# Kernel optimization log

Hardware: AMD Instinct MI355X
Metric: run time of the kernel (lower is better)

The kernel has to match this reference:

```python
import jax, jax.numpy as jnp
import numpy as np

DIM, E, H, HS = 2048, 8, 1408, 2816
B, S = 4, 2048


def setup_inputs() -> dict:
    key = jax.random.key(0)
    ks = jax.random.split(key, 12)
    sc = 0.02
    return {
        "x": jax.random.normal(ks[0], (B, S, DIM), jnp.float32),
        "gate_w": jax.random.normal(ks[1], (E, DIM), jnp.float32) * sc,
        "gate_b": jnp.zeros((E,), jnp.float32),
        "w1": jax.random.normal(ks[2], (E, H, DIM), jnp.float32) * sc,
        "b1": jnp.zeros((E, H), jnp.float32),
        "w3": jax.random.normal(ks[3], (E, H, DIM), jnp.float32) * sc,
        "b3": jnp.zeros((E, H), jnp.float32),
        "w2": jax.random.normal(ks[4], (E, DIM, H), jnp.float32) * sc,
        "b2": jnp.zeros((E, DIM), jnp.float32),
        "sh_gate": jax.random.normal(ks[5], (HS, DIM), jnp.float32) * sc,
        "sh_up": jax.random.normal(ks[6], (HS, DIM), jnp.float32) * sc,
        "sh_down": jax.random.normal(ks[7], (DIM, HS), jnp.float32) * sc,
        "top_k": 2,
    }


def reference(x, gate_w, gate_b, w1, b1, w3, b3, w2, b2, sh_gate, sh_up, sh_down, top_k):
    shape = x.shape
    xt = x.reshape(-1, DIM)                       # [T, D]
    T = xt.shape[0]

    # Router: softmax -> top-k (bias is None so gathered weights == topk probs)
    logits = xt @ gate_w.T + gate_b               # [T, E]
    scores = jax.nn.softmax(logits, axis=-1)
    topk_w, topk_idx = jax.lax.top_k(scores, top_k)  # [T, K]
    # combine weights per (token, expert); topk indices are distinct per row
    combine = jnp.zeros((T, E), xt.dtype).at[jnp.arange(T)[:, None], topk_idx].add(topk_w)

    # Routed experts: dense batched SwiGLU over all experts, weighted combine.
    g = jax.nn.silu(jnp.einsum("td,ehd->teh", xt, w1) + b1)  # [T, E, H]
    u = jnp.einsum("td,ehd->teh", xt, w3) + b3               # [T, E, H]
    hw = (g * u) * combine[:, :, None]                        # weight before down-proj
    routed = jnp.einsum("teh,edh->td", hw, w2) + combine @ b2  # [T, D]

    # Shared expert (bias-free SwiGLU)
    shared = (jax.nn.silu(xt @ sh_gate.T) * (xt @ sh_up.T)) @ sh_down.T

    return (shared + routed).reshape(shape)
```

## Files before the change

kernel.cpp:

```cpp
#include <hip/hip_runtime.h>
#include <stdint.h>

#define DIM  2048
#define NEXP 8
#define NH   1408
#define NHS  2816
#define NT   8192
#define NA   (NT*2)

typedef unsigned short u16;
typedef short bf16x8 __attribute__((ext_vector_type(8)));
typedef float f32x4 __attribute__((ext_vector_type(4)));

typedef __attribute__((address_space(1))) const uint32_t gas_u32;
typedef __attribute__((address_space(3))) uint32_t las_u32;

__device__ __forceinline__ u16 f2bf(float f) {
  uint32_t x = __builtin_bit_cast(uint32_t, f);
  x += 0x7FFFu + ((x >> 16) & 1u);
  return (u16)(x >> 16);
}

__device__ __forceinline__ void gload_lds16(const void* g, void* l) {
  __builtin_amdgcn_global_load_lds((gas_u32*)g, (las_u32*)l, 16, 0, 0);
}

struct alignas(16) US8 { u16 u[8]; };

__global__ __launch_bounds__(256) void convert_kernel(const float* __restrict__ src,
                                                      u16* __restrict__ dst, int n8) {
  int i = blockIdx.x * 256 + threadIdx.x;
  if (i >= n8) return;
  const float4* s = (const float4*)src + (size_t)i * 2;
  float4 a = s[0], b = s[1];
  US8 r;
  r.u[0]=f2bf(a.x); r.u[1]=f2bf(a.y); r.u[2]=f2bf(a.z); r.u[3]=f2bf(a.w);
  r.u[4]=f2bf(b.x); r.u[5]=f2bf(b.y); r.u[6]=f2bf(b.z); r.u[7]=f2bf(b.w);
  *((US8*)dst + i) = r;
}

__global__ void zero_counts(int* counts) { if (threadIdx.x < NEXP) counts[threadIdx.x] = 0; }

__global__ __launch_bounds__(64) void router_kernel(const float* __restrict__ x,
    const float* __restrict__ gw, const float* __restrict__ gb,
    int* __restrict__ tope, float* __restrict__ topw, int* __restrict__ counts) {
  const int t = blockIdx.x;
  const int lane = threadIdx.x;
  const float4* xr = (const float4*)(x + (size_t)t * DIM);
  float4 xv[8];
  #pragma unroll
  for (int j = 0; j < 8; j++) xv[j] = xr[j * 64 + lane];
  float p[NEXP];
  #pragma unroll
  for (int e = 0; e < NEXP; e++) {
    const float4* gr = (const float4*)(gw + (size_t)e * DIM);
    float s = 0.f;
    #pragma unroll
    for (int j = 0; j < 8; j++) {
      float4 g = gr[j * 64 + lane];
      s += xv[j].x*g.x + xv[j].y*g.y + xv[j].z*g.z + xv[j].w*g.w;
    }
    p[e] = s;
  }
  #pragma unroll
  for (int off = 32; off > 0; off >>= 1) {
    #pragma unroll
    for (int e = 0; e < NEXP; e++) p[e] += __shfl_xor(p[e], off);
  }
  if (lane == 0) {
    float pr[NEXP];
    float mx = -1e30f;
    #pragma unroll
    for (int e = 0; e < NEXP; e++) { p[e] += gb[e]; mx = fmaxf(mx, p[e]); }
    float den = 0.f;
    #pragma unroll
    for (int e = 0; e < NEXP; e++) { pr[e] = __expf(p[e] - mx); den += pr[e]; }
    float inv = 1.f / den;
    #pragma unroll
    for (int e = 0; e < NEXP; e++) pr[e] *= inv;
    int e0 = 0;
    #pragma unroll
    for (int e = 1; e < NEXP; e++) if (pr[e] > pr[e0]) e0 = e;
    int e1 = (e0 == 0) ? 1 : 0;
    #pragma unroll
    for (int e = 0; e < NEXP; e++) { if (e != e0 && pr[e] > pr[e1]) e1 = e; }
    tope[t*2]   = e0; tope[t*2+1] = e1;
    topw[t*2]   = pr[e0]; topw[t*2+1] = pr[e1];
    atomicAdd(&counts[e0], 1); atomicAdd(&counts[e1], 1);
  }
}

__global__ void scan_kernel(const int* __restrict__ counts, int* __restrict__ offsets,
                            int* __restrict__ cursor) {
  if (threadIdx.x == 0) {
    int s = 0;
    for (int e = 0; e < NEXP; e++) { offsets[e] = s; cursor[e] = s; s += counts[e]; }
    offsets[NEXP] = s;
  }
}

__global__ __launch_bounds__(256) void assign_kernel(const int* __restrict__ tope,
    const float* __restrict__ topw, int* __restrict__ cursor,
    int* __restrict__ ptok, float* __restrict__ pw) {
  int t = blockIdx.x * 256 + threadIdx.x;
  if (t >= NT) return;
  #pragma unroll
  for (int k = 0; k < 2; k++) {
    int e = tope[t*2+k];
    int pos = atomicAdd(&cursor[e], 1);
    ptok[pos] = t;
    pw[pos]   = topw[t*2+k];
  }
}

template<bool ROUTED>
__global__ __launch_bounds__(256, 2) void gemm_up(
    const u16* __restrict__ X,
    const u16* __restrict__ Wg,
    const u16* __restrict__ Wu,
    const float* __restrict__ Bg,
    const float* __restrict__ Bu,
    u16* __restrict__ Hout,
    const int* __restrict__ offsets,
    const int* __restrict__ ptok,
    const float* __restrict__ pw,
    int Nfeat)
{
  const int nt = blockIdx.x;
  const int mt = blockIdx.y;
  int e = 0, seg = 0, cnt = NT;
  if (ROUTED) {
    e = blockIdx.z;
    seg = offsets[e];
    cnt = offsets[e+1] - seg;
    if (mt * 128 >= cnt) return;
  }
  const int m0 = mt * 128;
  const int tid = threadIdx.x;
  const int wave = tid >> 6, lane = tid & 63;

  __shared__ u16 sA[128*64];
  __shared__ u16 sBg[64*64];
  __shared__ u16 sBu[64*64];
  char* sAc  = (char*)sA;
  char* sBgc = (char*)sBg;
  char* sBuc = (char*)sBu;

  const u16* aSrc[4];
  #pragma unroll
  for (int j = 0; j < 4; j++) {
    int c = j * 256 + tid;
    int row = c >> 3, gch = (c & 7) ^ (row & 7);
    int r = m0 + row;
    size_t srow;
    if (ROUTED) { r = (r < cnt) ? r : (cnt - 1); srow = (size_t)ptok[seg + r]; }
    else        { srow = (size_t)r; }
    aSrc[j] = X + srow * DIM + gch * 8;
  }
  const size_t wOff = ROUTED ? (size_t)e * Nfeat * DIM : 0;
  const u16 *bgSrc[2], *buSrc[2];
  #pragma unroll
  for (int j = 0; j < 2; j++) {
    int c = j * 256 + tid;
    int row = c >> 3, gch = (c & 7) ^ (row & 7);
    bgSrc[j] = Wg + wOff + (size_t)(nt * 64 + row) * DIM + gch * 8;
    buSrc[j] = Wu + wOff + (size_t)(nt * 64 + row) * DIM + gch * 8;
  }

  f32x4 accg[4][2], accu[4][2];
  #pragma unroll
  for (int m = 0; m < 4; m++)
    #pragma unroll
    for (int n = 0; n < 2; n++) { accg[m][n] = (f32x4){0,0,0,0}; accu[m][n] = (f32x4){0,0,0,0}; }

  const int wr = (wave >> 1) * 64;
  const int wc = (wave & 1) * 32;
  const int lr = lane & 15, kg = lane >> 4;
  int aOff[4], bOff[2];
  #pragma unroll
  for (int m = 0; m < 4; m++) { int row = wr + m*16 + lr; aOff[m] = row*128 + ((kg ^ (row & 7)) & 7) * 16; }
  #pragma unroll
  for (int n = 0; n < 2; n++) { int row = wc + n*16 + lr; bOff[n] = row*128 + ((kg ^ (row & 7)) & 7) * 16; }

  for (int k0 = 0; k0 < DIM; k0 += 64) {
    __syncthreads();
    #pragma unroll
    for (int j = 0; j < 4; j++) gload_lds16(aSrc[j] + k0, sAc + j*4096 + wave*1024);
    #pragma unroll
    for (int j = 0; j < 2; j++) {
      gload_lds16(bgSrc[j] + k0, sBgc + j*4096 + wave*1024);
      gload_lds16(buSrc[j] + k0, sBuc + j*4096 + wave*1024);
    }
    __syncthreads();
    bf16x8 af[4][2], bgf[2][2], buf2[2][2];
    #pragma unroll
    for (int m = 0; m < 4; m++) {
      af[m][0] = *(const bf16x8*)(sAc + aOff[m]);
      af[m][1] = *(const bf16x8*)(sAc + (aOff[m] ^ 64));
    }
    #pragma unroll
    for (int n = 0; n < 2; n++) {
      bgf[n][0]  = *(const bf16x8*)(sBgc + bOff[n]);
      bgf[n][1]  = *(const bf16x8*)(sBgc + (bOff[n] ^ 64));
      buf2[n][0] = *(const bf16x8*)(sBuc + bOff[n]);
      buf2[n][1] = *(const bf16x8*)(sBuc + (bOff[n] ^ 64));
    }
    #pragma unroll
    for (int kk = 0; kk < 2; kk++)
      #pragma unroll
      for (int m = 0; m < 4; m++)
        #pragma unroll
        for (int n = 0; n < 2; n++) {
          accg[m][n] = __builtin_amdgcn_mfma_f32_16x16x32_bf16(af[m][kk], bgf[n][kk],  accg[m][n], 0, 0, 0);
          accu[m][n] = __builtin_amdgcn_mfma_f32_16x16x32_bf16(af[m][kk], buf2[n][kk], accu[m][n], 0, 0, 0);
        }
  }

  const int col0 = nt * 64 + wc;
  #pragma unroll
  for (int m = 0; m < 4; m++) {
    #pragma unroll
    for (int n = 0; n < 2; n++) {
      #pragma unroll
      for (int i = 0; i < 4; i++) {
        int rl = wr + m*16 + (lane >> 4) * 4 + i;
        int gr = m0 + rl;
        if (ROUTED && gr >= cnt) continue;
        int col = col0 + n*16 + (lane & 15);
        float g = accg[m][n][i];
        float u = accu[m][n][i];
        float scale = 1.f;
        size_t orow;
        if (ROUTED) {
          int ai = seg + gr;
          scale = pw[ai];
          g += Bg[e * Nfeat + col];
          u += Bu[e * Nfeat + col];
          orow = (size_t)ai;
        } else {
          orow = (size_t)gr;
        }
        float s = g / (1.f + __expf(-g));
        Hout[orow * (size_t)Nfeat + col] = f2bf(s * u * scale);
      }
    }
  }
}

template<bool ROUTED>
__global__ __launch_bounds__(256, 2) void gemm_down(
    const u16* __restrict__ Hin,
    const u16* __restrict__ W,
    const float* __restrict__ B2,
    float* __restrict__ Out,
    const int* __restrict__ offsets,
    const int* __restrict__ ptok,
    const float* __restrict__ pw,
    int Kdim)
{
  const int nt = blockIdx.x;
  const int mt = blockIdx.y;
  int e = 0, seg = 0, cnt = NT;
  if (ROUTED) {
    e = blockIdx.z;
    seg = offsets[e];
    cnt = offsets[e+1] - seg;
    if (mt * 128 >= cnt) return;
  }
  const int m0 = mt * 128;
  const int tid = threadIdx.x;
  const int wave = tid >> 6, lane = tid & 63;

  __shared__ u16 sA[128*64];
  __shared__ u16 sB[128*64];
  char* sAc = (char*)sA;
  char* sBc = (char*)sB;

  const u16* aSrc[4]; const u16* bSrc[4];
  #pragma unroll
  for (int j = 0; j < 4; j++) {
    int c = j * 256 + tid;
    int row = c >> 3, gch = (c & 7) ^ (row & 7);
    int r = m0 + row;
    size_t arow;
    if (ROUTED) { r = (r < cnt) ? r : (cnt - 1); arow = (size_t)(seg + r); }
    else        { arow = (size_t)r; }
    aSrc[j] = Hin + arow * (size_t)Kdim + gch * 8;
    size_t brow = (size_t)(ROUTED ? e * DIM : 0) + nt * 128 + row;
    bSrc[j] = W + brow * (size_t)Kdim + gch * 8;
  }

  f32x4 acc[4][4];
  #pragma unroll
  for (int m = 0; m < 4; m++)
    #pragma unroll
    for (int n = 0; n < 4; n++) acc[m][n] = (f32x4){0,0,0,0};

  const int wr = (wave >> 1) * 64, wc = (wave & 1) * 64;
  const int lr = lane & 15, kg = lane >> 4;
  int aOff[4], bOff[4];
  #pragma unroll
  for (int m = 0; m < 4; m++) { int row = wr + m*16 + lr; aOff[m] = row*128 + ((kg ^ (row & 7)) & 7) * 16; }
  #pragma unroll
  for (int n = 0; n < 4; n++) { int row = wc + n*16 + lr; bOff[n] = row*128 + ((kg ^ (row & 7)) & 7) * 16; }

  for (int k0 = 0; k0 < Kdim; k0 += 64) {
    __syncthreads();
    #pragma unroll
    for (int j = 0; j < 4; j++) {
      gload_lds16(aSrc[j] + k0, sAc + j*4096 + wave*1024);
      gload_lds16(bSrc[j] + k0, sBc + j*4096 + wave*1024);
    }
    __syncthreads();
    bf16x8 af[4][2], bf[4][2];
    #pragma unroll
    for (int m = 0; m < 4; m++) {
      af[m][0] = *(const bf16x8*)(sAc + aOff[m]);
      af[m][1] = *(const bf16x8*)(sAc + (aOff[m] ^ 64));
    }
    #pragma unroll
    for (int n = 0; n < 4; n++) {
      bf[n][0] = *(const bf16x8*)(sBc + bOff[n]);
      bf[n][1] = *(const bf16x8*)(sBc + (bOff[n] ^ 64));
    }
    #pragma unroll
    for (int kk = 0; kk < 2; kk++)
      #pragma unroll
      for (int m = 0; m < 4; m++)
        #pragma unroll
        for (int n = 0; n < 4; n++)
          acc[m][n] = __builtin_amdgcn_mfma_f32_16x16x32_bf16(af[m][kk], bf[n][kk], acc[m][n], 0, 0, 0);
  }

  const int col0 = nt * 128 + wc;
  #pragma unroll
  for (int m = 0; m < 4; m++) {
    #pragma unroll
    for (int n = 0; n < 4; n++) {
      #pragma unroll
      for (int i = 0; i < 4; i++) {
        int rl = wr + m*16 + (lane >> 4) * 4 + i;
        int gr = m0 + rl;
        int col = col0 + n*16 + (lane & 15);
        float v = acc[m][n][i];
        if (ROUTED) {
          if (gr < cnt) {
            int ai = seg + gr;
            int token = ptok[ai];
            float w = pw[ai];
            atomicAdd(Out + (size_t)token * DIM + col, v + w * B2[e * DIM + col]);
          }
        } else {
          Out[(size_t)gr * DIM + col] = v;
        }
      }
    }
  }
}

extern "C" void kernel_launch(void* const* d_in, const int* in_sizes, int n_in,
                              void* d_out, int out_size, void* d_ws, size_t ws_size,
                              hipStream_t stream) {
  (void)in_sizes; (void)n_in; (void)out_size; (void)ws_size;
  const float* x      = (const float*)d_in[0];
  const float* gate_w = (const float*)d_in[1];
  const float* gate_b = (const float*)d_in[2];
  const float* w1     = (const float*)d_in[3];
  const float* b1     = (const float*)d_in[4];
  const float* w3     = (const float*)d_in[5];
  const float* b3     = (const float*)d_in[6];
  const float* w2     = (const float*)d_in[7];
  const float* b2     = (const float*)d_in[8];
  const float* shg    = (const float*)d_in[9];
  const float* shu    = (const float*)d_in[10];
  const float* shd    = (const float*)d_in[11];
  float* out = (float*)d_out;

  char* ws = (char*)d_ws;
  size_t off = 0;
  auto alloc = [&](size_t bytes) -> void* {
    void* p = ws + off;
    off += (bytes + 255) & ~(size_t)255;
    return p;
  };
  u16* xb    = (u16*)alloc((size_t)NT * DIM * 2);
  u16* w1b   = (u16*)alloc((size_t)NEXP * NH * DIM * 2);
  u16* w3b   = (u16*)alloc((size_t)NEXP * NH * DIM * 2);
  u16* w2b   = (u16*)alloc((size_t)NEXP * DIM * NH * 2);
  u16* shgb  = (u16*)alloc((size_t)NHS * DIM * 2);
  u16* shub  = (u16*)alloc((size_t)NHS * DIM * 2);
  u16* shdb  = (u16*)alloc((size_t)DIM * NHS * 2);
  u16* hsh   = (u16*)alloc((size_t)NT * NHS * 2);
  u16* hr    = (u16*)alloc((size_t)NA * NH * 2);
  int*   tope    = (int*)alloc(NT * 2 * 4);
  float* topw    = (float*)alloc(NT * 2 * 4);
  int*   ptok    = (int*)alloc(NA * 4);
  float* pw      = (float*)alloc(NA * 4);
  int*   counts  = (int*)alloc(64);
  int*   offsets = (int*)alloc(64);
  int*   cursor  = (int*)alloc(64);

  auto cvt = [&](const float* s, u16* d, size_t n) {
    int n8 = (int)(n / 8);
    convert_kernel<<<(n8 + 255) / 256, 256, 0, stream>>>(s, d, n8);
  };
  cvt(x,   xb,   (size_t)NT * DIM);
  cvt(w1,  w1b,  (size_t)NEXP * NH * DIM);
  cvt(w3,  w3b,  (size_t)NEXP * NH * DIM);
  cvt(w2,  w2b,  (size_t)NEXP * DIM * NH);
  cvt(shg, shgb, (size_t)NHS * DIM);
  cvt(shu, shub, (size_t)NHS * DIM);
  cvt(shd, shdb, (size_t)DIM * NHS);

  zero_counts<<<1, 64, 0, stream>>>(counts);
  router_kernel<<<NT, 64, 0, stream>>>(x, gate_w, gate_b, tope, topw, counts);
  scan_kernel<<<1, 1, 0, stream>>>(counts, offsets, cursor);
  assign_kernel<<<NT / 256, 256, 0, stream>>>(tope, topw, cursor, ptok, pw);

  gemm_up<false><<<dim3(NHS / 64, NT / 128, 1), 256, 0, stream>>>(
      xb, shgb, shub, nullptr, nullptr, hsh, nullptr, nullptr, nullptr, NHS);
  gemm_up<true><<<dim3(NH / 64, NT / 128, NEXP), 256, 0, stream>>>(
      xb, w1b, w3b, b1, b3, hr, offsets, ptok, pw, NH);
  gemm_down<false><<<dim3(DIM / 128, NT / 128, 1), 256, 0, stream>>>(
      hsh, shdb, nullptr, out, nullptr, nullptr, nullptr, NHS);
  gemm_down<true><<<dim3(DIM / 128, NT / 128, NEXP), 256, 0, stream>>>(
      hr, w2b, b2, out, offsets, ptok, pw, NH);
}
```

Before: 1.123 ms.

## Double-buffer LDS tiles in up/down GEMMs and fuse x conversion into router

```diff
diff --git a/kernel.cpp b/kernel.cpp
--- a/kernel.cpp
+++ b/kernel.cpp
@@ -26,6 +26,7 @@
 }
 
 struct alignas(16) US8 { u16 u[8]; };
+struct alignas(8)  US4 { u16 u[4]; };
 
 __global__ __launch_bounds__(256) void convert_kernel(const float* __restrict__ src,
                                                       u16* __restrict__ dst, int n8) {
@@ -43,6 +44,7 @@
 
 __global__ __launch_bounds__(64) void router_kernel(const float* __restrict__ x,
     const float* __restrict__ gw, const float* __restrict__ gb,
+    u16* __restrict__ xb,
     int* __restrict__ tope, float* __restrict__ topw, int* __restrict__ counts) {
   const int t = blockIdx.x;
   const int lane = threadIdx.x;
@@ -50,6 +52,14 @@
   float4 xv[8];
   #pragma unroll
   for (int j = 0; j < 8; j++) xv[j] = xr[j * 64 + lane];
+  US4* xrow = (US4*)(xb + (size_t)t * DIM);
+  #pragma unroll
+  for (int j = 0; j < 8; j++) {
+    US4 r4;
+    r4.u[0] = f2bf(xv[j].x); r4.u[1] = f2bf(xv[j].y);
+    r4.u[2] = f2bf(xv[j].z); r4.u[3] = f2bf(xv[j].w);
+    xrow[j * 64 + lane] = r4;
+  }
   float p[NEXP];
   #pragma unroll
   for (int e = 0; e < NEXP; e++) {
@@ -139,9 +149,9 @@
   const int tid = threadIdx.x;
   const int wave = tid >> 6, lane = tid & 63;
 
-  __shared__ u16 sA[128*64];
-  __shared__ u16 sBg[64*64];
-  __shared__ u16 sBu[64*64];
+  __shared__ u16 sA[2*128*64];
+  __shared__ u16 sBg[2*64*64];
+  __shared__ u16 sBu[2*64*64];
   char* sAc  = (char*)sA;
   char* sBgc = (char*)sBg;
   char* sBuc = (char*)sBu;
@@ -182,28 +192,34 @@
   #pragma unroll
   for (int n = 0; n < 2; n++) { int row = wc + n*16 + lr; bOff[n] = row*128 + ((kg ^ (row & 7)) & 7) * 16; }
 
-  for (int k0 = 0; k0 < DIM; k0 += 64) {
+#define STAGE_UP(b, kt) { int k0_ = (kt) * 64; \
+  _Pragma("unroll") for (int j = 0; j < 4; j++) \
+    gload_lds16(aSrc[j] + k0_, sAc + (b)*16384 + j*4096 + wave*1024); \
+  _Pragma("unroll") for (int j = 0; j < 2; j++) { \
+    gload_lds16(bgSrc[j] + k0_, sBgc + (b)*8192 + j*4096 + wave*1024); \
+    gload_lds16(buSrc[j] + k0_, sBuc + (b)*8192 + j*4096 + wave*1024); } }
+
+  const int NKT = DIM / 64;
+  STAGE_UP(0, 0);
+  for (int t = 0; t < NKT; t++) {
     __syncthreads();
-    #pragma unroll
-    for (int j = 0; j < 4; j++) gload_lds16(aSrc[j] + k0, sAc + j*4096 + wave*1024);
-    #pragma unroll
-    for (int j = 0; j < 2; j++) {
-      gload_lds16(bgSrc[j] + k0, sBgc + j*4096 + wave*1024);
-      gload_lds16(buSrc[j] + k0, sBuc + j*4096 + wave*1024);
-    }
-    __syncthreads();
+    const int b = t & 1;
+    if (t + 1 < NKT) STAGE_UP(b ^ 1, t + 1);
+    const char* sa = sAc  + b * 16384;
+    const char* sg = sBgc + b * 8192;
+    const char* su = sBuc + b * 8192;
     bf16x8 af[4][2], bgf[2][2], buf2[2][2];
     #pragma unroll
     for (int m = 0; m < 4; m++) {
-      af[m][0] = *(const bf16x8*)(sAc + aOff[m]);
-      af[m][1] = *(const bf16x8*)(sAc + (aOff[m] ^ 64));
+      af[m][0] = *(const bf16x8*)(sa + aOff[m]);
+      af[m][1] = *(const bf16x8*)(sa + (aOff[m] ^ 64));
     }
     #pragma unroll
     for (int n = 0; n < 2; n++) {
-      bgf[n][0]  = *(const bf16x8*)(sBgc + bOff[n]);
-      bgf[n][1]  = *(const bf16x8*)(sBgc + (bOff[n] ^ 64));
-      buf2[n][0] = *(const bf16x8*)(sBuc + bOff[n]);
-      buf2[n][1] = *(const bf16x8*)(sBuc + (bOff[n] ^ 64));
+      bgf[n][0]  = *(const bf16x8*)(sg + bOff[n]);
+      bgf[n][1]  = *(const bf16x8*)(sg + (bOff[n] ^ 64));
+      buf2[n][0] = *(const bf16x8*)(su + bOff[n]);
+      buf2[n][1] = *(const bf16x8*)(su + (bOff[n] ^ 64));
     }
     #pragma unroll
     for (int kk = 0; kk < 2; kk++)
@@ -215,6 +231,7 @@
           accu[m][n] = __builtin_amdgcn_mfma_f32_16x16x32_bf16(af[m][kk], buf2[n][kk], accu[m][n], 0, 0, 0);
         }
   }
+#undef STAGE_UP
 
   const int col0 = nt * 64 + wc;
   #pragma unroll
@@ -271,8 +288,8 @@
   const int tid = threadIdx.x;
   const int wave = tid >> 6, lane = tid & 63;
 
-  __shared__ u16 sA[128*64];
-  __shared__ u16 sB[128*64];
+  __shared__ u16 sA[2*128*64];
+  __shared__ u16 sB[2*128*64];
   char* sAc = (char*)sA;
   char* sBc = (char*)sB;
 
@@ -304,24 +321,29 @@
   #pragma unroll
   for (int n = 0; n < 4; n++) { int row = wc + n*16 + lr; bOff[n] = row*128 + ((kg ^ (row & 7)) & 7) * 16; }
 
-  for (int k0 = 0; k0 < Kdim; k0 += 64) {
+#define STAGE_DN(b, kt) { int k0_ = (kt) * 64; \
+  _Pragma("unroll") for (int j = 0; j < 4; j++) { \
+    gload_lds16(aSrc[j] + k0_, sAc + (b)*16384 + j*4096 + wave*1024); \
+    gload_lds16(bSrc[j] + k0_, sBc + (b)*16384 + j*4096 + wave*1024); } }
+
+  const int NKT = Kdim / 64;
+  STAGE_DN(0, 0);
+  for (int t = 0; t < NKT; t++) {
     __syncthreads();
-    #pragma unroll
-    for (int j = 0; j < 4; j++) {
-      gload_lds16(aSrc[j] + k0, sAc + j*4096 + wave*1024);
-      gload_lds16(bSrc[j] + k0, sBc + j*4096 + wave*1024);
-    }
-    __syncthreads();
+    const int b = t & 1;
+    if (t + 1 < NKT) STAGE_DN(b ^ 1, t + 1);
+    const char* sa = sAc + b * 16384;
+    const char* sb = sBc + b * 16384;
     bf16x8 af[4][2], bf[4][2];
     #pragma unroll
     for (int m = 0; m < 4; m++) {
-      af[m][0] = *(const bf16x8*)(sAc + aOff[m]);
-      af[m][1] = *(const bf16x8*)(sAc + (aOff[m] ^ 64));
+      af[m][0] = *(const bf16x8*)(sa + aOff[m]);
+      af[m][1] = *(const bf16x8*)(sa + (aOff[m] ^ 64));
     }
     #pragma unroll
     for (int n = 0; n < 4; n++) {
-      bf[n][0] = *(const bf16x8*)(sBc + bOff[n]);
-      bf[n][1] = *(const bf16x8*)(sBc + (bOff[n] ^ 64));
+      bf[n][0] = *(const bf16x8*)(sb + bOff[n]);
+      bf[n][1] = *(const bf16x8*)(sb + (bOff[n] ^ 64));
     }
     #pragma unroll
     for (int kk = 0; kk < 2; kk++)
@@ -331,6 +353,7 @@
         for (int n = 0; n < 4; n++)
           acc[m][n] = __builtin_amdgcn_mfma_f32_16x16x32_bf16(af[m][kk], bf[n][kk], acc[m][n], 0, 0, 0);
   }
+#undef STAGE_DN
 
   const int col0 = nt * 128 + wc;
   #pragma unroll
@@ -404,7 +427,6 @@
     int n8 = (int)(n / 8);
     convert_kernel<<<(n8 + 255) / 256, 256, 0, stream>>>(s, d, n8);
   };
-  cvt(x,   xb,   (size_t)NT * DIM);
   cvt(w1,  w1b,  (size_t)NEXP * NH * DIM);
   cvt(w3,  w3b,  (size_t)NEXP * NH * DIM);
   cvt(w2,  w2b,  (size_t)NEXP * DIM * NH);
@@ -413,7 +435,7 @@
   cvt(shd, shdb, (size_t)DIM * NHS);
 
   zero_counts<<<1, 64, 0, stream>>>(counts);
-  router_kernel<<<NT, 64, 0, stream>>>(x, gate_w, gate_b, tope, topw, counts);
+  router_kernel<<<NT, 64, 0, stream>>>(x, gate_w, gate_b, xb, tope, topw, counts);
   scan_kernel<<<1, 1, 0, stream>>>(counts, offsets, cursor);
   assign_kernel<<<NT / 256, 256, 0, stream>>>(tope, topw, cursor, ptok, pw);
 
```

New measurement: 1.387 ms. 1.24x slower.

## Interleave gate/up weights and use 256x256 pipelined up-projection GEMM

Applied to the files above, without the earlier changes.

```diff
diff --git a/kernel.cpp b/kernel.cpp
--- a/kernel.cpp
+++ b/kernel.cpp
@@ -26,6 +26,7 @@
 }
 
 struct alignas(16) US8 { u16 u[8]; };
+struct alignas(8)  US4 { u16 u[4]; };
 
 __global__ __launch_bounds__(256) void convert_kernel(const float* __restrict__ src,
                                                       u16* __restrict__ dst, int n8) {
@@ -39,10 +40,24 @@
   *((US8*)dst + i) = r;
 }
 
+__global__ __launch_bounds__(256) void convert_ilv(const float* __restrict__ src,
+                                                   u16* __restrict__ dst, int n8, int par) {
+  int i = blockIdx.x * 256 + threadIdx.x;
+  if (i >= n8) return;
+  int row = i >> 8, c = i & 255;
+  const float4* s = (const float4*)src + (size_t)i * 2;
+  float4 a = s[0], b = s[1];
+  US8 r;
+  r.u[0]=f2bf(a.x); r.u[1]=f2bf(a.y); r.u[2]=f2bf(a.z); r.u[3]=f2bf(a.w);
+  r.u[4]=f2bf(b.x); r.u[5]=f2bf(b.y); r.u[6]=f2bf(b.z); r.u[7]=f2bf(b.w);
+  *((US8*)dst + (((size_t)(2*row + par)) << 8) + c) = r;
+}
+
 __global__ void zero_counts(int* counts) { if (threadIdx.x < NEXP) counts[threadIdx.x] = 0; }
 
 __global__ __launch_bounds__(64) void router_kernel(const float* __restrict__ x,
     const float* __restrict__ gw, const float* __restrict__ gb,
+    u16* __restrict__ xb,
     int* __restrict__ tope, float* __restrict__ topw, int* __restrict__ counts) {
   const int t = blockIdx.x;
   const int lane = threadIdx.x;
@@ -50,6 +65,14 @@
   float4 xv[8];
   #pragma unroll
   for (int j = 0; j < 8; j++) xv[j] = xr[j * 64 + lane];
+  US4* xrow = (US4*)(xb + (size_t)t * DIM);
+  #pragma unroll
+  for (int j = 0; j < 8; j++) {
+    US4 r4;
+    r4.u[0] = f2bf(xv[j].x); r4.u[1] = f2bf(xv[j].y);
+    r4.u[2] = f2bf(xv[j].z); r4.u[3] = f2bf(xv[j].w);
+    xrow[j * 64 + lane] = r4;
+  }
   float p[NEXP];
   #pragma unroll
   for (int e = 0; e < NEXP; e++) {
@@ -113,150 +136,157 @@
   }
 }
 
-template<bool ROUTED>
-__global__ __launch_bounds__(256, 2) void gemm_up(
-    const u16* __restrict__ X,
-    const u16* __restrict__ Wg,
-    const u16* __restrict__ Wu,
-    const float* __restrict__ Bg,
-    const float* __restrict__ Bu,
-    u16* __restrict__ Hout,
-    const int* __restrict__ offsets,
-    const int* __restrict__ ptok,
-    const float* __restrict__ pw,
-    int Nfeat)
+#define BAR() { asm volatile("" ::: "memory"); __builtin_amdgcn_s_barrier(); asm volatile("" ::: "memory"); }
+#define VM6 asm volatile("s_waitcnt vmcnt(6)" ::: "memory")
+#define VM0 asm volatile("s_waitcnt vmcnt(0)" ::: "memory")
+
+template<int EPI>
+__global__ __launch_bounds__(512, 2) void gemm8(
+    const u16* __restrict__ A, const u16* __restrict__ Bw, u16* __restrict__ Hout,
+    const float* __restrict__ biasG, const float* __restrict__ biasU,
+    const int* __restrict__ offsets, const int* __restrict__ ptok,
+    const float* __restrict__ pw, int M, int N, int K, int Hf)
 {
-  const int nt = blockIdx.x;
-  const int mt = blockIdx.y;
-  int e = 0, seg = 0, cnt = NT;
-  if (ROUTED) {
-    e = blockIdx.z;
-    seg = offsets[e];
-    cnt = offsets[e+1] - seg;
-    if (mt * 128 >= cnt) return;
-  }
-  const int m0 = mt * 128;
-  const int tid = threadIdx.x;
-  const int wave = tid >> 6, lane = tid & 63;
-
-  __shared__ u16 sA[128*64];
-  __shared__ u16 sBg[64*64];
-  __shared__ u16 sBu[64*64];
-  char* sAc  = (char*)sA;
-  char* sBgc = (char*)sBg;
-  char* sBuc = (char*)sBu;
-
-  const u16* aSrc[4];
-  #pragma unroll
-  for (int j = 0; j < 4; j++) {
-    int c = j * 256 + tid;
-    int row = c >> 3, gch = (c & 7) ^ (row & 7);
-    int r = m0 + row;
-    size_t srow;
-    if (ROUTED) { r = (r < cnt) ? r : (cnt - 1); srow = (size_t)ptok[seg + r]; }
-    else        { srow = (size_t)r; }
-    aSrc[j] = X + srow * DIM + gch * 8;
-  }
-  const size_t wOff = ROUTED ? (size_t)e * Nfeat * DIM : 0;
-  const u16 *bgSrc[2], *buSrc[2];
-  #pragma unroll
-  for (int j = 0; j < 2; j++) {
-    int c = j * 256 + tid;
-    int row = c >> 3, gch = (c & 7) ^ (row & 7);
-    bgSrc[j] = Wg + wOff + (size_t)(nt * 64 + row) * DIM + gch * 8;
-    buSrc[j] = Wu + wOff + (size_t)(nt * 64 + row) * DIM + gch * 8;
-  }
-
-  f32x4 accg[4][2], accu[4][2];
-  #pragma unroll
-  for (int m = 0; m < 4; m++)
-    #pragma unroll
-    for (int n = 0; n < 2; n++) { accg[m][n] = (f32x4){0,0,0,0}; accu[m][n] = (f32x4){0,0,0,0}; }
-
-  const int wr = (wave >> 1) * 64;
-  const int wc = (wave & 1) * 32;
-  const int lr = lane & 15, kg = lane >> 4;
-  int aOff[4], bOff[2];
-  #pragma unroll
-  for (int m = 0; m < 4; m++) { int row = wr + m*16 + lr; aOff[m] = row*128 + ((kg ^ (row & 7)) & 7) * 16; }
-  #pragma unroll
-  for (int n = 0; n < 2; n++) { int row = wc + n*16 + lr; bOff[n] = row*128 + ((kg ^ (row & 7)) & 7) * 16; }
-
-  for (int k0 = 0; k0 < DIM; k0 += 64) {
-    __syncthreads();
-    #pragma unroll
-    for (int j = 0; j < 4; j++) gload_lds16(aSrc[j] + k0, sAc + j*4096 + wave*1024);
-    #pragma unroll
-    for (int j = 0; j < 2; j++) {
-      gload_lds16(bgSrc[j] + k0, sBgc + j*4096 + wave*1024);
-      gload_lds16(buSrc[j] + k0, sBuc + j*4096 + wave*1024);
-    }
-    __syncthreads();
-    bf16x8 af[4][2], bgf[2][2], buf2[2][2];
-    #pragma unroll
-    for (int m = 0; m < 4; m++) {
-      af[m][0] = *(const bf16x8*)(sAc + aOff[m]);
-      af[m][1] = *(const bf16x8*)(sAc + (aOff[m] ^ 64));
-    }
-    #pragma unroll
-    for (int n = 0; n < 2; n++) {
-      bgf[n][0]  = *(const bf16x8*)(sBgc + bOff[n]);
-      bgf[n][1]  = *(const bf16x8*)(sBgc + (bOff[n] ^ 64));
-      buf2[n][0] = *(const bf16x8*)(sBuc + bOff[n]);
-      buf2[n][1] = *(const bf16x8*)(sBuc + (bOff[n] ^ 64));
-    }
-    #pragma unroll
-    for (int kk = 0; kk < 2; kk++)
+  constexpr bool SEG = (EPI == 1);
+  extern __shared__ char smem[];
+  const int nt = blockIdx.x, mt = blockIdx.y;
+  int e = 0, seg = 0, cnt = M;
+  if (SEG) { e = blockIdx.z; seg = offsets[e]; cnt = offsets[e+1] - seg; if (mt*256 >= cnt) return; }
+  const int tid = threadIdx.x, wave = tid >> 6, lane = tid & 63;
+  const int NKT = K >> 6;
+
+  const u16* Bp = Bw + (SEG ? (size_t)e * (size_t)N * K : (size_t)0);
+  const u16* sAp[2][2]; const u16* sBp[2][2];
+  {
+    const int trow = tid >> 3;
+    const int tch  = (tid & 7) ^ (trow & 7);
+    #pragma unroll
+    for (int h = 0; h < 2; h++)
       #pragma unroll
-      for (int m = 0; m < 4; m++)
-        #pragma unroll
-        for (int n = 0; n < 2; n++) {
-          accg[m][n] = __builtin_amdgcn_mfma_f32_16x16x32_bf16(af[m][kk], bgf[n][kk],  accg[m][n], 0, 0, 0);
-          accu[m][n] = __builtin_amdgcn_mfma_f32_16x16x32_bf16(af[m][kk], buf2[n][kk], accu[m][n], 0, 0, 0);
-        }
-  }
-
-  const int col0 = nt * 64 + wc;
-  #pragma unroll
-  for (int m = 0; m < 4; m++) {
-    #pragma unroll
-    for (int n = 0; n < 2; n++) {
+      for (int j = 0; j < 2; j++) {
+        int r = mt*256 + h*128 + j*64 + trow;
+        if (SEG) r = (r < cnt) ? r : (cnt - 1);
+        size_t arow = SEG ? (size_t)ptok[seg + r] : (size_t)r;
+        sAp[h][j] = A + arow * (size_t)K + tch * 8;
+        int br = nt*256 + h*128 + j*64 + trow;
+        sBp[h][j] = Bp + (size_t)br * K + tch * 8;
+      }
+  }
+
+  const int wm = wave >> 2, wn = wave & 3, hb = wn >> 1;
+  const int ln15 = lane & 15, kg = lane >> 4;
+  const int c0 = (kg ^ (ln15 & 7)) << 4;
+  const char* Ab0 = smem + ((0*2 + wm) << 14);
+  const char* Ab1 = smem + ((1*2 + wm) << 14);
+  const char* Bb0 = smem + 65536 + ((0*2 + hb) << 14);
+  const char* Bb1 = smem + 65536 + ((1*2 + hb) << 14);
+  const int arow0 = ln15 * 128;
+  const int brow0 = ((wn & 1) * 64 + ln15) * 128;
+
+  f32x4 acc[8][4];
+  #pragma unroll
+  for (int m = 0; m < 8; m++)
+    #pragma unroll
+    for (int n = 0; n < 4; n++) acc[m][n] = (f32x4){0,0,0,0};
+
+  bf16x8 fa[4][2], fb[4][2];
+
+#define STA(buf,h,kt) { size_t k_ = (size_t)(kt) * 64; \
+  gload_lds16(sAp[h][0] + k_, smem + (((buf)*2+(h))<<14) + wave*1024); \
+  gload_lds16(sAp[h][1] + k_, smem + (((buf)*2+(h))<<14) + 8192 + wave*1024); }
+#define STB(buf,h,kt) { size_t k_ = (size_t)(kt) * 64; \
+  gload_lds16(sBp[h][0] + k_, smem + 65536 + (((buf)*2+(h))<<14) + wave*1024); \
+  gload_lds16(sBp[h][1] + k_, smem + 65536 + (((buf)*2+(h))<<14) + 8192 + wave*1024); }
+#define LDFA(AB, qm) { _Pragma("unroll") for (int m_ = 0; m_ < 4; m_++) { \
+  const char* p_ = (AB) + (qm)*8192 + m_*2048 + arow0; \
+  fa[m_][0] = *(const bf16x8*)(p_ + c0); fa[m_][1] = *(const bf16x8*)(p_ + (c0 ^ 64)); } }
+#define LDFB(BB) { _Pragma("unroll") for (int n_ = 0; n_ < 4; n_++) { \
+  const char* p_ = (BB) + n_*2048 + brow0; \
+  fb[n_][0] = *(const bf16x8*)(p_ + c0); fb[n_][1] = *(const bf16x8*)(p_ + (c0 ^ 64)); } }
+#define PH(qm, n0) { __builtin_amdgcn_s_setprio(1); \
+  _Pragma("unroll") for (int kk_ = 0; kk_ < 2; kk_++) \
+  _Pragma("unroll") for (int m_ = 0; m_ < 4; m_++) \
+  _Pragma("unroll") for (int n_ = 0; n_ < 2; n_++) \
+    acc[(qm)*4+m_][(n0)+n_] = __builtin_amdgcn_mfma_f32_16x16x32_bf16( \
+        fa[m_][kk_], fb[(n0)+n_][kk_], acc[(qm)*4+m_][(n0)+n_], 0, 0, 0); \
+  __builtin_amdgcn_s_setprio(0); }
+
+  STB(0,0,0); STB(0,1,0); STA(0,0,0); STA(0,1,0);
+  STB(1,0,1); STB(1,1,1); STA(1,0,1);
+  VM6; BAR();
+
+  for (int t = 0; t < NKT; t += 2) {
+    const bool last = (t + 2 >= NKT);
+    LDFB(Bb0); LDFA(Ab0, 0);
+    STA(1,1,t+1);
+    PH(0,0);
+    BAR();
+    if (!last) STB(0,0,t+2);
+    PH(0,2);
+    BAR();
+    LDFA(Ab0, 1);
+    if (!last) STB(0,1,t+2);
+    PH(1,2);
+    BAR();
+    if (!last) { STA(0,0,t+2); VM6; } else { VM0; }
+    PH(1,0);
+    BAR();
+    LDFB(Bb1); LDFA(Ab1, 0);
+    if (!last) STA(0,1,t+2);
+    PH(0,0);
+    BAR();
+    if (!last) STB(1,0,t+3);
+    PH(0,2);
+    BAR();
+    LDFA(Ab1, 1);
+    if (!last) STB(1,1,t+3);
+    PH(1,2);
+    BAR();
+    if (!last) { STA(1,0,t+3); VM6; }
+    PH(1,0);
+    BAR();
+  }
+
+  #pragma unroll
+  for (int mi = 0; mi < 8; mi++) {
+    #pragma unroll
+    for (int ni = 0; ni < 4; ni++) {
+      int colC = nt*256 + wn*64 + ni*16 + ln15;
+      int h = colC >> 1;
+      int par = ln15 & 1;
       #pragma unroll
       for (int i = 0; i < 4; i++) {
-        int rl = wr + m*16 + (lane >> 4) * 4 + i;
-        int gr = m0 + rl;
-        if (ROUTED && gr >= cnt) continue;
-        int col = col0 + n*16 + (lane & 15);
-        float g = accg[m][n][i];
-        float u = accu[m][n][i];
-        float scale = 1.f;
-        size_t orow;
-        if (ROUTED) {
-          int ai = seg + gr;
-          scale = pw[ai];
-          g += Bg[e * Nfeat + col];
-          u += Bu[e * Nfeat + col];
-          orow = (size_t)ai;
+        float v = acc[mi][ni][i];
+        float v2 = __shfl_xor(v, 1);
+        float g = par ? v2 : v;
+        float uu = par ? v : v2;
+        int rr = mt*256 + wm*128 + mi*16 + kg*4 + i;
+        if (EPI == 1) { g += biasG[e*Hf + h]; uu += biasU[e*Hf + h]; }
+        float hv = (g / (1.f + __expf(-g))) * uu;
+        if (EPI == 0) {
+          if (par == 0) Hout[(size_t)rr * Hf + h] = f2bf(hv);
         } else {
-          orow = (size_t)gr;
+          if (par == 0 && rr < cnt) {
+            int ai = seg + rr;
+            Hout[(size_t)ai * Hf + h] = f2bf(hv * pw[ai]);
+          }
         }
-        float s = g / (1.f + __expf(-g));
-        Hout[orow * (size_t)Nfeat + col] = f2bf(s * u * scale);
       }
     }
   }
+#undef STA
+#undef STB
+#undef LDFA
+#undef LDFB
+#undef PH
 }
 
 template<bool ROUTED>
 __global__ __launch_bounds__(256, 2) void gemm_down(
-    const u16* __restrict__ Hin,
-    const u16* __restrict__ W,
-    const float* __restrict__ B2,
-    float* __restrict__ Out,
-    const int* __restrict__ offsets,
-    const int* __restrict__ ptok,
-    const float* __restrict__ pw,
-    int Kdim)
+    const u16* __restrict__ Hin, const u16* __restrict__ W,
+    const float* __restrict__ B2, float* __restrict__ Out,
+    const int* __restrict__ offsets, const int* __restrict__ ptok,
+    const float* __restrict__ pw, int Kdim)
 {
   const int nt = blockIdx.x;
   const int mt = blockIdx.y;
@@ -384,11 +414,9 @@
     return p;
   };
   u16* xb    = (u16*)alloc((size_t)NT * DIM * 2);
-  u16* w1b   = (u16*)alloc((size_t)NEXP * NH * DIM * 2);
-  u16* w3b   = (u16*)alloc((size_t)NEXP * NH * DIM * 2);
+  u16* wupr  = (u16*)alloc((size_t)NEXP * 2 * NH * DIM * 2);
   u16* w2b   = (u16*)alloc((size_t)NEXP * DIM * NH * 2);
-  u16* shgb  = (u16*)alloc((size_t)NHS * DIM * 2);
-  u16* shub  = (u16*)alloc((size_t)NHS * DIM * 2);
+  u16* wupsh = (u16*)alloc((size_t)2 * NHS * DIM * 2);
   u16* shdb  = (u16*)alloc((size_t)DIM * NHS * 2);
   u16* hsh   = (u16*)alloc((size_t)NT * NHS * 2);
   u16* hr    = (u16*)alloc((size_t)NA * NH * 2);
@@ -400,27 +428,35 @@
   int*   offsets = (int*)alloc(64);
   int*   cursor  = (int*)alloc(64);
 
+  (void)hipFuncSetAttribute((const void*)gemm8<0>, hipFuncAttributeMaxDynamicSharedMemorySize, 131072);
+  (void)hipFuncSetAttribute((const void*)gemm8<1>, hipFuncAttributeMaxDynamicSharedMemorySize, 131072);
+
   auto cvt = [&](const float* s, u16* d, size_t n) {
     int n8 = (int)(n / 8);
     convert_kernel<<<(n8 + 255) / 256, 256, 0, stream>>>(s, d, n8);
   };
-  cvt(x,   xb,   (size_t)NT * DIM);
-  cvt(w1,  w1b,  (size_t)NEXP * NH * DIM);
-  cvt(w3,  w3b,  (size_t)NEXP * NH * DIM);
-  cvt(w2,  w2b,  (size_t)NEXP * DIM * NH);
-  cvt(shg, shgb, (size_t)NHS * DIM);
-  cvt(shu, shub, (size_t)NHS * DIM);
-  cvt(shd, shdb, (size_t)DIM * NHS);
+  auto cvi = [&](const float* s, u16* d, size_t n, int par) {
+    int n8 = (int)(n / 8);
+    convert_ilv<<<(n8 + 255) / 256, 256, 0, stream>>>(s, d, n8, par);
+  };
+  cvi(w1,  wupr,  (size_t)NEXP * NH * DIM, 0);
+  cvi(w3,  wupr,  (size_t)NEXP * NH * DIM, 1);
+  cvt(w2,  w2b,   (size_t)NEXP * DIM * NH);
+  cvi(shg, wupsh, (size_t)NHS * DIM, 0);
+  cvi(shu, wupsh, (size_t)NHS * DIM, 1);
+  cvt(shd, shdb,  (size_t)DIM * NHS);
 
   zero_counts<<<1, 64, 0, stream>>>(counts);
-  router_kernel<<<NT, 64, 0, stream>>>(x, gate_w, gate_b, tope, topw, counts);
+  router_kernel<<<NT, 64, 0, stream>>>(x, gate_w, gate_b, xb, tope, topw, counts);
   scan_kernel<<<1, 1, 0, stream>>>(counts, offsets, cursor);
   assign_kernel<<<NT / 256, 256, 0, stream>>>(tope, topw, cursor, ptok, pw);
 
-  gemm_up<false><<<dim3(NHS / 64, NT / 128, 1), 256, 0, stream>>>(
-      xb, shgb, shub, nullptr, nullptr, hsh, nullptr, nullptr, nullptr, NHS);
-  gemm_up<true><<<dim3(NH / 64, NT / 128, NEXP), 256, 0, stream>>>(
-      xb, w1b, w3b, b1, b3, hr, offsets, ptok, pw, NH);
+  gemm8<0><<<dim3(2*NHS/256, NT/256, 1), 512, 131072, stream>>>(
+      xb, wupsh, hsh, nullptr, nullptr, nullptr, nullptr, nullptr,
+      NT, 2*NHS, DIM, NHS);
+  gemm8<1><<<dim3(2*NH/256, NT/256, NEXP), 512, 131072, stream>>>(
+      xb, wupr, hr, b1, b3, offsets, ptok, pw,
+      NT, 2*NH, DIM, NH);
   gemm_down<false><<<dim3(DIM / 128, NT / 128, 1), 256, 0, stream>>>(
       hsh, shdb, nullptr, out, nullptr, nullptr, nullptr, NHS);
   gemm_down<true><<<dim3(DIM / 128, NT / 128, NEXP), 256, 0, stream>>>(
```

New measurement: 1.188 ms. +5.7%, slower.
